# Performance work log

Hardware: AMD Instinct MI355X
Metric: run time of the kernel (lower is better)

## Reference

```python
import jax, jax.numpy as jnp
import numpy as np


def setup_inputs() -> dict:
    key = jax.random.key(0)
    ks = jax.random.split(key, 8)
    B, L, d_model = 2, 4096, 1024
    d_inner, d_state, d_conv, dt_rank = 2048, 16, 4, 64
    f = jnp.float32
    g = lambda k, shape, scale: jax.random.normal(k, shape, dtype=f) * scale
    # dt bias init: inverse-softplus of dt ~ U[log 1e-3, log 1e-1] (as in Mamba)
    dt = jnp.exp(jax.random.uniform(ks[5], (d_inner,), f) * (np.log(0.1) - np.log(0.001)) + np.log(0.001))
    dt = jnp.clip(dt, 1e-4, None)
    inv_dt = dt + jnp.log(-jnp.expm1(-dt))
    A_log = jnp.log(jnp.broadcast_to(jnp.arange(1, d_state + 1, dtype=f), (d_inner, d_state)))
    return {
        "hidden_states": jax.random.normal(ks[0], (B, L, d_model), f),
        "in_proj_w": g(ks[1], (2 * d_inner, d_model), 0.02),
        "conv_w": g(ks[2], (d_inner, d_conv), 0.1),
        "conv_b": jnp.zeros((d_inner,), f),
        "x_proj_w": g(ks[3], (dt_rank + 2 * d_state, d_inner), 0.02),
        "dt_proj_w": g(ks[4], (d_inner, dt_rank), dt_rank ** -0.5),
        "dt_proj_b": inv_dt,
        "A_log": A_log,
        "D": jnp.ones((d_inner,), f),
        "out_proj_w": g(ks[6], (d_model, d_inner), 0.02),
    }


def reference(hidden_states, in_proj_w, conv_w, conv_b, x_proj_w, dt_proj_w, dt_proj_b, A_log, D, out_proj_w):
    B_, L, _ = hidden_states.shape
    d_inner, d_conv = conv_w.shape
    dt_rank = dt_proj_w.shape[1]
    d_state = A_log.shape[1]

    # input projection -> x, z gates (B, L, d_inner) each
    xz = jnp.einsum('bld,ed->ble', hidden_states, in_proj_w)
    x, z = jnp.split(xz, 2, axis=-1)

    # causal depthwise conv1d over time + SiLU
    xc = jnp.transpose(x, (0, 2, 1))                       # (B, d_inner, L)
    kern = conv_w[:, None, :]                              # (O=d_inner, I/g=1, W)
    xc = jax.lax.conv_general_dilated(
        xc, kern, window_strides=(1,), padding=[(d_conv - 1, 0)],
        dimension_numbers=('NCH', 'OIH', 'NCH'), feature_group_count=d_inner)
    xc = xc + conv_b[None, :, None]
    x = jax.nn.silu(jnp.transpose(xc, (0, 2, 1)))          # (B, L, d_inner)

    # data-dependent SSM parameters
    x_dbl = jnp.einsum('bld,kd->blk', x, x_proj_w)         # (B, L, dt_rank+2n)
    dt, Bm, Cm = jnp.split(x_dbl, [dt_rank, dt_rank + d_state], axis=-1)
    dt = jnp.einsum('blr,dr->bld', dt, dt_proj_w)
    dt = jax.nn.softplus(dt + dt_proj_b)                   # delta_softplus + delta_bias
    A = -jnp.exp(A_log)                                    # (d_inner, d_state)

    # selective scan over the sequence dim; carry h: (B, d_inner, d_state)
    def step(h, inp):
        x_t, dt_t, B_t, C_t = inp                          # (B,d) (B,d) (B,n) (B,n)
        dA = jnp.exp(dt_t[..., None] * A)                  # (B, d, n)
        h = h * dA + (dt_t * x_t)[..., None] * B_t[:, None, :]
        y = jnp.einsum('bdn,bn->bd', h, C_t)
        return h, y

    h0 = jnp.zeros((B_, d_inner, d_state), x.dtype)
    xs = (jnp.transpose(x, (1, 0, 2)), jnp.transpose(dt, (1, 0, 2)),
          jnp.transpose(Bm, (1, 0, 2)), jnp.transpose(Cm, (1, 0, 2)))
    _, ys = jax.lax.scan(step, h0, xs)                     # ys: (L, B, d_inner)

    y = jnp.transpose(ys, (1, 0, 2)) + x * D               # skip via D
    y = y * jax.nn.silu(z)                                 # gate
    return jnp.einsum('bld,od->blo', y, out_proj_w)        # (B, L, d_model)
```

## Files before the change

kernel.cpp:

```cpp
#include <hip/hip_runtime.h>
#include <cmath>

#define CH 64
#define NC 64

typedef __bf16 bf16_t;
typedef __attribute__((ext_vector_type(8))) __bf16 bf16x8;
typedef __attribute__((ext_vector_type(4))) __bf16 bf16x4;
typedef __attribute__((ext_vector_type(4))) float f32x4;

#define GLOAD_LDS16(gp, lp)                                                     \
    __builtin_amdgcn_global_load_lds(                                           \
        (const __attribute__((address_space(1))) unsigned int*)(uintptr_t)(gp), \
        (__attribute__((address_space(3))) unsigned int*)(uintptr_t)(lp),       \
        16, 0, 0)

__global__ __launch_bounds__(256) void split5n(
    const float* __restrict__ a, bf16_t* __restrict__ ah, int n4a,
    const float* __restrict__ b, bf16_t* __restrict__ bh, int n4b,
    const float* __restrict__ c, bf16_t* __restrict__ ch, bf16_t* __restrict__ cl, int n4c,
    const float* __restrict__ d, bf16_t* __restrict__ dh, bf16_t* __restrict__ dl, int n4d,
    const float* __restrict__ e, bf16_t* __restrict__ eh, int n4e)
{
    int i = blockIdx.x * 256 + threadIdx.x;
    if (i < n4a) {
        const float4 v = ((const float4*)a)[i];
        bf16x4 hv = {(bf16_t)v.x, (bf16_t)v.y, (bf16_t)v.z, (bf16_t)v.w};
        ((bf16x4*)ah)[i] = hv;
        return;
    }
    i -= n4a;
    if (i < n4b) {
        const float4 v = ((const float4*)b)[i];
        bf16x4 hv = {(bf16_t)v.x, (bf16_t)v.y, (bf16_t)v.z, (bf16_t)v.w};
        ((bf16x4*)bh)[i] = hv;
        return;
    }
    i -= n4b;
    if (i >= n4c + n4d) {
        i -= n4c + n4d;
        if (i < n4e) {
            const float4 v = ((const float4*)e)[i];
            bf16x4 hv = {(bf16_t)v.x, (bf16_t)v.y, (bf16_t)v.z, (bf16_t)v.w};
            ((bf16x4*)eh)[i] = hv;
        }
        return;
    }
    const float* src; bf16_t* hp; bf16_t* lp;
    if (i < n4c) { src = c; hp = ch; lp = cl; }
    else         { i -= n4c; src = d; hp = dh; lp = dl; }

    const float4 v = ((const float4*)src)[i];
    const bf16_t h0 = (bf16_t)v.x, h1 = (bf16_t)v.y,
                 h2 = (bf16_t)v.z, h3 = (bf16_t)v.w;
    bf16x4 hv = {h0, h1, h2, h3};
    bf16x4 lv = {(bf16_t)(v.x - (float)h0), (bf16_t)(v.y - (float)h1),
                 (bf16_t)(v.z - (float)h2), (bf16_t)(v.w - (float)h3)};
    ((bf16x4*)hp)[i] = hv;
    ((bf16x4*)lp)[i] = lv;
}

__global__ __launch_bounds__(256) void add8_split(
    const float* __restrict__ p, float* __restrict__ o,
    bf16_t* __restrict__ dth, bf16_t* __restrict__ dtl,
    int n4, size_t stride4)
{
    const int i = blockIdx.x * 256 + threadIdx.x;
    if (i >= n4) return;
    float4 s = make_float4(0.f, 0.f, 0.f, 0.f);
#pragma unroll
    for (int k = 0; k < 8; ++k) {
        const float4 v = ((const float4*)p)[(size_t)k * stride4 + i];
        s.x += v.x; s.y += v.y; s.z += v.z; s.w += v.w;
    }
    ((float4*)o)[i] = s;

    const int col4 = i % 24;
    if (col4 < 16) {
        const int row = i / 24;
        const bf16_t h0 = (bf16_t)s.x, h1 = (bf16_t)s.y,
                     h2 = (bf16_t)s.z, h3 = (bf16_t)s.w;
        bf16x4 hv = {h0, h1, h2, h3};
        bf16x4 lv = {(bf16_t)(s.x - (float)h0), (bf16_t)(s.y - (float)h1),
                     (bf16_t)(s.z - (float)h2), (bf16_t)(s.w - (float)h3)};
        ((bf16x4*)dth)[(size_t)row * 16 + col4] = hv;
        ((bf16x4*)dtl)[(size_t)row * 16 + col4] = lv;
    }
}

__global__ __launch_bounds__(256) void in_proj_fused1(
    const bf16_t* __restrict__ Ah, const bf16_t* __restrict__ Wh,
    bf16_t* __restrict__ X, bf16_t* __restrict__ Z, int Ktot)
{
    __shared__ __align__(16) bf16_t Ash[128 * 32];
    __shared__ __align__(16) bf16_t Bsh[128 * 32];

    const int tid  = threadIdx.x;
    const int lane = tid & 63;
    const int w    = tid >> 6;
    const int wr   = (w >> 1) * 64;
    const int wc   = (w & 1) * 64;
    const int bm   = blockIdx.x * 128;
    const int by   = blockIdx.y;
    const int bnW  = by * 128;
    const int l16  = lane & 15;
    const int lhi  = lane >> 4;

    f32x4 acc[4][4];
#pragma unroll
    for (int i = 0; i < 4; ++i)
#pragma unroll
        for (int j = 0; j < 4; ++j)
#pragma unroll
            for (int r = 0; r < 4; ++r) acc[i][j][r] = 0.f;

    const int srow0 = tid >> 2;
    const int sks   = (tid & 3) << 3;
    const int ldsb0 = tid * 16;

    for (int k0 = 0; k0 < Ktot; k0 += 32) {
        __syncthreads();
#pragma unroll
        for (int call = 0; call < 2; ++call) {
            const int row = srow0 + call * 64;
            const int wb  = ldsb0 + call * 4096;
            GLOAD_LDS16(Ah + (size_t)(bm + row) * Ktot + k0 + sks, (char*)Ash + wb);
            GLOAD_LDS16(Wh + (size_t)(bnW + row) * Ktot + k0 + sks, (char*)Bsh + wb);
        }
        __syncthreads();

        bf16x8 af[4], bfr[4];
#pragma unroll
        for (int f = 0; f < 4; ++f) {
            af[f]  = *(const bf16x8*)&Ash[(wr + f * 16 + l16) * 32 + lhi * 8];
            bfr[f] = *(const bf16x8*)&Bsh[(wc + f * 16 + l16) * 32 + lhi * 8];
        }
#pragma unroll
        for (int fm = 0; fm < 4; ++fm)
#pragma unroll
            for (int fn = 0; fn < 4; ++fn)
                acc[fm][fn] = __builtin_amdgcn_mfma_f32_16x16x32_bf16(
                    af[fm], bfr[fn], acc[fm][fn], 0, 0, 0);
    }

    bf16_t* outp = (by < 16) ? X : Z;
    const int bnC = ((by < 16) ? by : (by - 16)) * 128;
#pragma unroll
    for (int fm = 0; fm < 4; ++fm) {
        const int row0 = bm + wr + fm * 16 + lhi * 4;
#pragma unroll
        for (int fn = 0; fn < 4; ++fn) {
            const int col = bnC + wc + fn * 16 + l16;
#pragma unroll
            for (int r = 0; r < 4; ++r)
                outp[(size_t)(row0 + r) * 2048 + col] = (bf16_t)acc[fm][fn][r];
        }
    }
}

__global__ __launch_bounds__(256) void gemm_mfma3dt(
    const bf16_t* __restrict__ Ah, const bf16_t* __restrict__ Al,
    const bf16_t* __restrict__ Bh, const bf16_t* __restrict__ Bl,
    bf16_t* __restrict__ C, const float* __restrict__ bias,
    int Ktot, int ldc)
{
    __shared__ __align__(16) bf16_t Ash[128 * 32];
    __shared__ __align__(16) bf16_t Asl[128 * 32];
    __shared__ __align__(16) bf16_t Bsh[128 * 32];
    __shared__ __align__(16) bf16_t Bsl[128 * 32];

    const int tid  = threadIdx.x;
    const int lane = tid & 63;
    const int w    = tid >> 6;
    const int wr   = (w >> 1) * 64;
    const int wc   = (w & 1) * 64;
    const int bm   = blockIdx.x * 128;
    const int bn   = blockIdx.y * 128;
    const int l16  = lane & 15;
    const int lhi  = lane >> 4;

    f32x4 acc[4][4];
#pragma unroll
    for (int i = 0; i < 4; ++i)
#pragma unroll
        for (int j = 0; j < 4; ++j)
#pragma unroll
            for (int r = 0; r < 4; ++r) acc[i][j][r] = 0.f;

    const int srow0 = tid >> 2;
    const int sks   = (tid & 3) << 3;
    const int ldsb0 = tid * 16;

    for (int k0 = 0; k0 < Ktot; k0 += 32) {
        __syncthreads();
#pragma unroll
        for (int call = 0; call < 2; ++call) {
            const int row = srow0 + call * 64;
            const int wb  = ldsb0 + call * 4096;
            const size_t aoff = (size_t)(bm + row) * Ktot + k0 + sks;
            const size_t boff = (size_t)(bn + row) * Ktot + k0 + sks;
            GLOAD_LDS16(Ah + aoff, (char*)Ash + wb);
            GLOAD_LDS16(Al + aoff, (char*)Asl + wb);
            GLOAD_LDS16(Bh + boff, (char*)Bsh + wb);
            GLOAD_LDS16(Bl + boff, (char*)Bsl + wb);
        }
        __syncthreads();

        bf16x8 ah[4], al[4], bh[4], bl[4];
#pragma unroll
        for (int f = 0; f < 4; ++f) {
            const int ar = (wr + f * 16 + l16) * 32 + lhi * 8;
            const int br = (wc + f * 16 + l16) * 32 + lhi * 8;
            ah[f] = *(const bf16x8*)&Ash[ar];
            al[f] = *(const bf16x8*)&Asl[ar];
            bh[f] = *(const bf16x8*)&Bsh[br];
            bl[f] = *(const bf16x8*)&Bsl[br];
        }
#pragma unroll
        for (int fm = 0; fm < 4; ++fm)
#pragma unroll
            for (int fn = 0; fn < 4; ++fn) {
                acc[fm][fn] = __builtin_amdgcn_mfma_f32_16x16x32_bf16(
                    ah[fm], bh[fn], acc[fm][fn], 0, 0, 0);
                acc[fm][fn] = __builtin_amdgcn_mfma_f32_16x16x32_bf16(
                    al[fm], bh[fn], acc[fm][fn], 0, 0, 0);
                acc[fm][fn] = __builtin_amdgcn_mfma_f32_16x16x32_bf16(
                    ah[fm], bl[fn], acc[fm][fn], 0, 0, 0);
            }
    }

#pragma unroll
    for (int fm = 0; fm < 4; ++fm) {
        const int row0 = bm + wr + fm * 16 + lhi * 4;
#pragma unroll
        for (int fn = 0; fn < 4; ++fn) {
            const int col = bn + wc + fn * 16 + l16;
#pragma unroll
            for (int r = 0; r < 4; ++r) {
                float v = acc[fm][fn][r] + bias[col];
                v = (v > 20.f) ? v : log1pf(expf(v));
                C[(size_t)(row0 + r) * ldc + col] = (bf16_t)v;
            }
        }
    }
}

__global__ __launch_bounds__(256) void gemm_mfma2x(
    const bf16_t* __restrict__ Ah,
    const bf16_t* __restrict__ Bh, const bf16_t* __restrict__ Bl,
    float* __restrict__ C, int Ktot, int Ksplit, size_t partStride)
{
    __shared__ __align__(16) bf16_t Ash[128 * 32];
    __shared__ __align__(16) bf16_t Bsh[128 * 32];
    __shared__ __align__(16) bf16_t Bsl[128 * 32];

    const int tid  = threadIdx.x;
    const int lane = tid & 63;
    const int w    = tid >> 6;
    const int wr   = (w >> 1) * 64;
    const int wc   = (w & 1) * 64;
    const int bm   = blockIdx.x * 128;
    const int l16  = lane & 15;
    const int lhi  = lane >> 4;

    f32x4 acc[4][4];
#pragma unroll
    for (int i = 0; i < 4; ++i)
#pragma unroll
        for (int j = 0; j < 4; ++j)
#pragma unroll
            for (int r = 0; r < 4; ++r) acc[i][j][r] = 0.f;

    const int srow0 = tid >> 2;
    const int sks   = (tid & 3) << 3;
    const int ldsb0 = tid * 16;

    const int kBeg = blockIdx.z * Ksplit;
    const int kEnd = kBeg + Ksplit;

    for (int k0 = kBeg; k0 < kEnd; k0 += 32) {
        __syncthreads();
#pragma unroll
        for (int call = 0; call < 2; ++call) {
            const int row  = srow0 + call * 64;
            const int brow = (row < 96) ? row : 95;
            const int wb   = ldsb0 + call * 4096;
            const size_t aoff = (size_t)(bm + row) * Ktot + k0 + sks;
            const size_t boff = (size_t)brow * Ktot + k0 + sks;
            GLOAD_LDS16(Ah + aoff, (char*)Ash + wb);
            GLOAD_LDS16(Bh + boff, (char*)Bsh + wb);
            GLOAD_LDS16(Bl + boff, (char*)Bsl + wb);
        }
        __syncthreads();

        bf16x8 ah[4], bh[4], bl[4];
#pragma unroll
        for (int f = 0; f < 4; ++f) {
            const int ar = (wr + f * 16 + l16) * 32 + lhi * 8;
            const int br = (wc + f * 16 + l16) * 32 + lhi * 8;
            ah[f] = *(const bf16x8*)&Ash[ar];
            bh[f] = *(const bf16x8*)&Bsh[br];
            bl[f] = *(const bf16x8*)&Bsl[br];
        }
#pragma unroll
        for (int fm = 0; fm < 4; ++fm)
#pragma unroll
            for (int fn = 0; fn < 4; ++fn) {
                acc[fm][fn] = __builtin_amdgcn_mfma_f32_16x16x32_bf16(
                    ah[fm], bh[fn], acc[fm][fn], 0, 0, 0);
                acc[fm][fn] = __builtin_amdgcn_mfma_f32_16x16x32_bf16(
                    ah[fm], bl[fn], acc[fm][fn], 0, 0, 0);
            }
    }

    float* Cp = C + (size_t)blockIdx.z * partStride;
#pragma unroll
    for (int fm = 0; fm < 4; ++fm) {
        const int row0 = bm + wr + fm * 16 + lhi * 4;
#pragma unroll
        for (int fn = 0; fn < 4; ++fn) {
            const int col = wc + fn * 16 + l16;
            if (col < 96) {
#pragma unroll
                for (int r = 0; r < 4; ++r)
                    Cp[(size_t)(row0 + r) * 96 + col] = acc[fm][fn][r];
            }
        }
    }
}

__global__ __launch_bounds__(256) void gemm_mfma1o128(
    const bf16_t* __restrict__ Ah, const bf16_t* __restrict__ Bh,
    float* __restrict__ C, int K, int ldc)
{
    __shared__ __align__(16) bf16_t Ash[128 * 32];
    __shared__ __align__(16) bf16_t Bsh[128 * 32];

    const int tid  = threadIdx.x;
    const int lane = tid & 63;
    const int w    = tid >> 6;
    const int wr   = (w >> 1) * 64;
    const int wc   = (w & 1) * 64;
    const int bm   = blockIdx.x * 128;
    const int bn   = blockIdx.y * 128;
    const int l16  = lane & 15;
    const int lhi  = lane >> 4;

    f32x4 acc[4][4];
#pragma unroll
    for (int i = 0; i < 4; ++i)
#pragma unroll
        for (int j = 0; j < 4; ++j)
#pragma unroll
            for (int r = 0; r < 4; ++r) acc[i][j][r] = 0.f;

    const int srow0 = tid >> 2;
    const int sks   = (tid & 3) << 3;
    const int ldsb0 = tid * 16;

    for (int k0 = 0; k0 < K; k0 += 32) {
        __syncthreads();
#pragma unroll
        for (int call = 0; call < 2; ++call) {
            const int row = srow0 + call * 64;
            const int wb  = ldsb0 + call * 4096;
            GLOAD_LDS16(Ah + (size_t)(bm + row) * K + k0 + sks, (char*)Ash + wb);
            GLOAD_LDS16(Bh + (size_t)(bn + row) * K + k0 + sks, (char*)Bsh + wb);
        }
        __syncthreads();

        bf16x8 af[4], bfr[4];
#pragma unroll
        for (int f = 0; f < 4; ++f) {
            af[f]  = *(const bf16x8*)&Ash[(wr + f * 16 + l16) * 32 + lhi * 8];
            bfr[f] = *(const bf16x8*)&Bsh[(wc + f * 16 + l16) * 32 + lhi * 8];
        }
#pragma unroll
        for (int fm = 0; fm < 4; ++fm)
#pragma unroll
            for (int fn = 0; fn < 4; ++fn)
                acc[fm][fn] = __builtin_amdgcn_mfma_f32_16x16x32_bf16(
                    af[fm], bfr[fn], acc[fm][fn], 0, 0, 0);
    }

#pragma unroll
    for (int fm = 0; fm < 4; ++fm) {
        const int row0 = bm + wr + fm * 16 + lhi * 4;
#pragma unroll
        for (int fn = 0; fn < 4; ++fn) {
            const int col = bn + wc + fn * 16 + l16;
#pragma unroll
            for (int r = 0; r < 4; ++r)
                C[(size_t)(row0 + r) * ldc + col] = acc[fm][fn][r];
        }
    }
}

__global__ __launch_bounds__(256) void conv_silu8s(
    const bf16_t* __restrict__ xin, const float* __restrict__ w,
    const float* __restrict__ bias,
    bf16_t* __restrict__ xh,
    int L, int D)
{
    const long long e8 = (long long)blockIdx.x * 256 + threadIdx.x;
    const int Dq = D >> 3;
    const int dq = (int)(e8 % Dq);
    const long long bl = e8 / Dq;
    const int l = (int)(bl % L);
    const int d = dq << 3;
    const long long base = bl * D + d;

    float t0[8], t1[8], t2[8], t3[8];
    {
        const bf16x8 v = *(const bf16x8*)&xin[base];
#pragma unroll
        for (int j = 0; j < 8; ++j) t0[j] = (float)v[j];
    }
    if (l >= 1) { const bf16x8 v = *(const bf16x8*)&xin[base - D];
#pragma unroll
        for (int j = 0; j < 8; ++j) t1[j] = (float)v[j];
    } else { for (int j = 0; j < 8; ++j) t1[j] = 0.f; }
    if (l >= 2) { const bf16x8 v = *(const bf16x8*)&xin[base - 2 * D];
#pragma unroll
        for (int j = 0; j < 8; ++j) t2[j] = (float)v[j];
    } else { for (int j = 0; j < 8; ++j) t2[j] = 0.f; }
    if (l >= 3) { const bf16x8 v = *(const bf16x8*)&xin[base - 3 * D];
#pragma unroll
        for (int j = 0; j < 8; ++j) t3[j] = (float)v[j];
    } else { for (int j = 0; j < 8; ++j) t3[j] = 0.f; }

    bf16x8 hv;
#pragma unroll
    for (int j = 0; j < 8; ++j) {
        const float4 wv = *(const float4*)&w[(d + j) * 4];
        float acc = bias[d + j];
        acc = fmaf(wv.w, t0[j], acc);
        acc = fmaf(wv.z, t1[j], acc);
        acc = fmaf(wv.y, t2[j], acc);
        acc = fmaf(wv.x, t3[j], acc);
        const float o = acc / (1.f + __expf(-acc));
        hv[j] = (bf16_t)o;
    }
    *(bf16x8*)&xh[base] = hv;
}

__global__ __launch_bounds__(256) void scan_local2(
    const bf16_t* __restrict__ xh,
    const bf16_t* __restrict__ dtb,
    const float* __restrict__ xdbl,  const float* __restrict__ A_log,
    float* __restrict__ Sbuf, float* __restrict__ Pbuf)
{
    __shared__ float Bs[CH][16];

    const int d = blockIdx.x * 256 + threadIdx.x;
    const int c = blockIdx.y;
    const int b = blockIdx.z;
    const long long rowBase = (long long)b * 4096 + (long long)c * CH;

    {
        const int e = threadIdx.x;
        const int i = e >> 2, j = (e & 3) << 2;
        *(float4*)&Bs[i][j] = *(const float4*)&xdbl[(rowBase + i) * 96 + 64 + j];
    }
    __syncthreads();

    float a[16], S[16];
#pragma unroll
    for (int n = 0; n < 16; ++n) {
        a[n] = -__expf(A_log[d * 16 + n]);
        S[n] = 0.f;
    }
    float sumdt = 0.f;

    for (int i = 0; i < CH; ++i) {
        const long long row = rowBase + i;
        const float dtv = (float)dtb[row * 2048 + d];
        const float xv  = (float)xh[row * 2048 + d];
        const float u   = dtv * xv;
        sumdt += dtv;
#pragma unroll
        for (int n = 0; n < 16; ++n) {
            const float dA = __expf(dtv * a[n]);
            S[n] = fmaf(S[n], dA, u * Bs[i][n]);
        }
    }

    const size_t base = ((((size_t)b * NC + c) * 2048) + d) * 16;
#pragma unroll
    for (int k = 0; k < 4; ++k) {
        *(float4*)&Sbuf[base + k * 4] =
            make_float4(S[k*4], S[k*4+1], S[k*4+2], S[k*4+3]);
        *(float4*)&Pbuf[base + k * 4] =
            make_float4(__expf(sumdt * a[k*4]),   __expf(sumdt * a[k*4+1]),
                        __expf(sumdt * a[k*4+2]), __expf(sumdt * a[k*4+3]));
    }
}

__global__ __launch_bounds__(256) void scan_chunk_prefix(
    float* __restrict__ Sbuf, const float* __restrict__ Pbuf)
{
    const int tid = blockIdx.x * 256 + threadIdx.x;
    const int b  = tid >> 15;
    const int dn = tid & 32767;

    float H = 0.f;
    for (int c = 0; c < NC; ++c) {
        const size_t idx = ((size_t)b * NC + c) * 32768 + dn;
        const float S = Sbuf[idx];
        const float P = Pbuf[idx];
        Sbuf[idx] = H;
        H = fmaf(P, H, S);
    }
}

__global__ __launch_bounds__(256) void scan_final2(
    const bf16_t* __restrict__ xh,
    const bf16_t* __restrict__ dtb,
    const float* __restrict__ xdbl,  const float* __restrict__ A_log,
    const float* __restrict__ Dp,    const bf16_t* __restrict__ z,
    const float* __restrict__ Hbuf,  bf16_t* __restrict__ y)
{
    __shared__ float BCs[CH][32];

    const int d = blockIdx.x * 256 + threadIdx.x;
    const int c = blockIdx.y;
    const int b = blockIdx.z;
    const long long rowBase = (long long)b * 4096 + (long long)c * CH;

#pragma unroll
    for (int k = 0; k < 2; ++k) {
        const int e = k * 256 + threadIdx.x;
        const int i = e >> 3, j = (e & 7) << 2;
        *(float4*)&BCs[i][j] = *(const float4*)&xdbl[(rowBase + i) * 96 + 64 + j];
    }
    __syncthreads();

    float a[16], h[16];
    const size_t hbase = ((((size_t)b * NC + c) * 2048) + d) * 16;
#pragma unroll
    for (int k = 0; k < 4; ++k) {
        const float4 hv = *(const float4*)&Hbuf[hbase + k * 4];
        h[k*4] = hv.x; h[k*4+1] = hv.y; h[k*4+2] = hv.z; h[k*4+3] = hv.w;
    }
#pragma unroll
    for (int n = 0; n < 16; ++n) a[n] = -__expf(A_log[d * 16 + n]);
    const float Dv = Dp[d];

    for (int i = 0; i < CH; ++i) {
        const long long row = rowBase + i;
        const float dtv = (float)dtb[row * 2048 + d];
        const float xv  = (float)xh[row * 2048 + d];
        const float u   = dtv * xv;
        float acc = 0.f;
#pragma unroll
        for (int n = 0; n < 16; ++n) {
            const float dA = __expf(dtv * a[n]);
            h[n] = fmaf(h[n], dA, u * BCs[i][n]);
            acc  = fmaf(h[n], BCs[i][16 + n], acc);
        }
        const float zv = (float)z[row * 2048 + d];
        float yv = acc + xv * Dv;
        yv = yv * (zv / (1.f + __expf(-zv)));
        y[row * 2048 + d] = (bf16_t)yv;
    }
}

extern "C" void kernel_launch(void* const* d_in, const int* in_sizes, int n_in,
                              void* d_out, int out_size, void* d_ws, size_t ws_size,
                              hipStream_t stream)
{
    const float* hidden     = (const float*)d_in[0];
    const float* in_proj_w  = (const float*)d_in[1];
    const float* conv_w     = (const float*)d_in[2];
    const float* conv_b     = (const float*)d_in[3];
    const float* x_proj_w   = (const float*)d_in[4];
    const float* dt_proj_w  = (const float*)d_in[5];
    const float* dt_proj_b  = (const float*)d_in[6];
    const float* A_log      = (const float*)d_in[7];
    const float* Dvec       = (const float*)d_in[8];
    const float* out_proj_w = (const float*)d_in[9];
    float* out = (float*)d_out;

    const int L = 4096, dinner = 2048, dmodel = 1024;
    const int M = 2 * L;

    float* z     = (float*)d_ws;
    float* xraw  = z     + (size_t)M * dinner;
    float* xconv = xraw  + (size_t)M * dinner;
    float* xdbl  = xconv + (size_t)M * dinner;
    float* Sbuf  = xdbl  + (size_t)M * 96;

    bf16_t* w1_h  = (bf16_t*)Sbuf;
    bf16_t* hid_h = (bf16_t*)xconv;
    bf16_t* zb    = (bf16_t*)z;
    bf16_t* Xb    = (bf16_t*)xraw;
    bf16_t* xc_h  = (bf16_t*)xconv;
    float*  xp_part = xraw;
    bf16_t* dtb  = (bf16_t*)xraw;
    bf16_t* dth  = (bf16_t*)Sbuf;
    bf16_t* dtl  = dth + (size_t)M * 64;
    bf16_t* wdh  = (bf16_t*)out;
    bf16_t* wdl  = wdh + (size_t)dinner * 64;
    bf16_t* xpwh = (bf16_t*)xdbl;
    bf16_t* xpwl = xpwh + (size_t)96 * dinner;
    bf16_t* w2_h = zb + (size_t)M * dinner;
    float*  Pbuf = (float*)(w2_h + (size_t)dmodel * dinner);

    const int n4a = M * dmodel / 4;
    const int n4b = 2 * dinner * dmodel / 4;
    const int n4c = dinner * 64 / 4;
    const int n4d = 96 * dinner / 4;
    const int n4e = dmodel * dinner / 4;
    split5n<<<(n4a + n4b + n4c + n4d + n4e + 255) / 256, 256, 0, stream>>>(
        hidden, hid_h, n4a,
        in_proj_w, w1_h, n4b,
        dt_proj_w, wdh, wdl, n4c,
        x_proj_w, xpwh, xpwl, n4d,
        out_proj_w, w2_h, n4e);

    in_proj_fused1<<<dim3(M / 128, 32), 256, 0, stream>>>(
        hid_h, w1_h, Xb, zb, dmodel);

    conv_silu8s<<<(M * (long long)dinner / 8) / 256, 256, 0, stream>>>(
        Xb, conv_w, conv_b, xc_h, L, dinner);

    gemm_mfma2x<<<dim3(M / 128, 1, 8), 256, 0, stream>>>(
        xc_h, xpwh, xpwl, xp_part, dinner, dinner / 8, (size_t)M * 96);
    add8_split<<<(M * 96 / 4 + 255) / 256, 256, 0, stream>>>(
        xp_part, xdbl, dth, dtl, M * 96 / 4, (size_t)M * 96 / 4);

    gemm_mfma3dt<<<dim3(M / 128, 2048 / 128), 256, 0, stream>>>(
        dth, dtl, wdh, wdl, dtb, dt_proj_b, 64, 2048);

    scan_local2<<<dim3(dinner / 256, NC, 2), 256, 0, stream>>>(
        xc_h, dtb, xdbl, A_log, Sbuf, Pbuf);
    scan_chunk_prefix<<<256, 256, 0, stream>>>(Sbuf, Pbuf);
    scan_final2<<<dim3(dinner / 256, NC, 2), 256, 0, stream>>>(
        xc_h, dtb, xdbl, A_log, Dvec, zb, Sbuf, xc_h);

    gemm_mfma1o128<<<dim3(M / 128, 1024 / 128), 256, 0, stream>>>(
        xc_h, w2_h, out, dinner, 1024);
}
```

Baseline: 439.3 us.

## Rewrite in_proj GEMM as 256x256 double-buffered 8-wave phased kernel

Replaces the 128x128 single-buffered in_proj GEMM with a 256x256 tile, 512-thread kernel. It double-buffers LDS with K=64 steps, prefetching the next tile while MFMAs run, and uses an XOR swizzle to avoid LDS bank conflicts. Compute is split into four barrier-separated phases with s_setprio so waves interleave loads and MFMA. The aim is to raise MFMA utilization and hide global-load latency, at the cost of 128KB of LDS, single-block occupancy, and more barriers.

Measured after the change: 426.0 us. 1.03x faster.

```diff
diff --git a/kernel.cpp b/kernel.cpp
--- a/kernel.cpp
+++ b/kernel.cpp
@@ -14,6 +14,8 @@
         (const __attribute__((address_space(1))) unsigned int*)(uintptr_t)(gp), \
         (__attribute__((address_space(3))) unsigned int*)(uintptr_t)(lp),       \
         16, 0, 0)
+
+#define SCHED_FENCE() __builtin_amdgcn_sched_barrier(0)
 
 __global__ __launch_bounds__(256) void split5n(
     const float* __restrict__ a, bf16_t* __restrict__ ah, int n4a,
@@ -88,69 +90,168 @@
     }
 }
 
-__global__ __launch_bounds__(256) void in_proj_fused1(
+__global__ __launch_bounds__(512, 1) void in_proj_8ph(
     const bf16_t* __restrict__ Ah, const bf16_t* __restrict__ Wh,
     bf16_t* __restrict__ X, bf16_t* __restrict__ Z, int Ktot)
 {
-    __shared__ __align__(16) bf16_t Ash[128 * 32];
-    __shared__ __align__(16) bf16_t Bsh[128 * 32];
+    __shared__ __align__(16) bf16_t lds[2][2][2][128 * 64];
 
     const int tid  = threadIdx.x;
     const int lane = tid & 63;
-    const int w    = tid >> 6;
-    const int wr   = (w >> 1) * 64;
-    const int wc   = (w & 1) * 64;
-    const int bm   = blockIdx.x * 128;
-    const int by   = blockIdx.y;
-    const int bnW  = by * 128;
+    const int wid  = tid >> 6;
+    const int wm   = wid >> 2;
+    const int wn   = wid & 3;
     const int l16  = lane & 15;
     const int lhi  = lane >> 4;
 
-    f32x4 acc[4][4];
-#pragma unroll
-    for (int i = 0; i < 4; ++i)
+    const int bm  = blockIdx.x * 256;
+    const int bnW = blockIdx.y * 256;
+
+    const int srow = tid >> 3;
+    const int scol = (tid & 7) * 8;
+    const int sflip = (srow & 4) << 2;
+
+    f32x4 acc[8][4];
+#pragma unroll
+    for (int i = 0; i < 8; ++i)
 #pragma unroll
         for (int j = 0; j < 4; ++j)
 #pragma unroll
             for (int r = 0; r < 4; ++r) acc[i][j][r] = 0.f;
 
-    const int srow0 = tid >> 2;
-    const int sks   = (tid & 3) << 3;
-    const int ldsb0 = tid * 16;
-
-    for (int k0 = 0; k0 < Ktot; k0 += 32) {
-        __syncthreads();
-#pragma unroll
-        for (int call = 0; call < 2; ++call) {
-            const int row = srow0 + call * 64;
-            const int wb  = ldsb0 + call * 4096;
-            GLOAD_LDS16(Ah + (size_t)(bm + row) * Ktot + k0 + sks, (char*)Ash + wb);
-            GLOAD_LDS16(Wh + (size_t)(bnW + row) * Ktot + k0 + sks, (char*)Bsh + wb);
-        }
-        __syncthreads();
-
-        bf16x8 af[4], bfr[4];
-#pragma unroll
-        for (int f = 0; f < 4; ++f) {
-            af[f]  = *(const bf16x8*)&Ash[(wr + f * 16 + l16) * 32 + lhi * 8];
-            bfr[f] = *(const bf16x8*)&Bsh[(wc + f * 16 + l16) * 32 + lhi * 8];
-        }
-#pragma unroll
-        for (int fm = 0; fm < 4; ++fm)
-#pragma unroll
-            for (int fn = 0; fn < 4; ++fn)
-                acc[fm][fn] = __builtin_amdgcn_mfma_f32_16x16x32_bf16(
-                    af[fm], bfr[fn], acc[fm][fn], 0, 0, 0);
-    }
-
-    bf16_t* outp = (by < 16) ? X : Z;
-    const int bnC = ((by < 16) ? by : (by - 16)) * 128;
-#pragma unroll
-    for (int fm = 0; fm < 4; ++fm) {
-        const int row0 = bm + wr + fm * 16 + lhi * 4;
+    const int NT = Ktot >> 6;
+
+    auto STAGE_TILE = [&](int pbuf, int kt) {
+        const int kc = kt * 64 + (scol ^ sflip);
+#pragma unroll
+        for (int h = 0; h < 2; ++h) {
+#pragma unroll
+            for (int j = 0; j < 2; ++j) {
+                const int row = h * 128 + j * 64 + srow;
+                char* da = (char*)&lds[pbuf][0][h][0] + (j * 512 + tid) * 16;
+                char* db = (char*)&lds[pbuf][1][h][0] + (j * 512 + tid) * 16;
+                GLOAD_LDS16(Ah + (size_t)(bm  + row) * Ktot + kc, da);
+                GLOAD_LDS16(Wh + (size_t)(bnW + row) * Ktot + kc, db);
+            }
+        }
+    };
+
+    const int rflip = (l16 & 4) << 2;
+    auto A_FRAG = [&](int p, int fm, int kk) -> bf16x8 {
+        return *(const bf16x8*)&lds[p][0][wm]
+            [(fm * 16 + l16) * 64 + ((kk * 32 + lhi * 8) ^ rflip)];
+    };
+    auto B_FRAG = [&](int p, int fn, int kk) -> bf16x8 {
+        return *(const bf16x8*)&lds[p][1][wn >> 1]
+            [((wn & 1) * 64 + fn * 16 + l16) * 64 + ((kk * 32 + lhi * 8) ^ rflip)];
+    };
+
+    STAGE_TILE(0, 0);
+    SCHED_FENCE();
+    asm volatile("s_waitcnt vmcnt(0)" ::: "memory");
+    __builtin_amdgcn_s_barrier();
+    SCHED_FENCE();
+
+    for (int kt = 0; kt < NT; ++kt) {
+        const int p  = kt & 1;
+        const int pn = p ^ 1;
+        bf16x8 a0[4][2], a1[4][2], b0[2][2], b1[2][2];
+
+#pragma unroll
+        for (int f = 0; f < 4; ++f)
+#pragma unroll
+            for (int kk = 0; kk < 2; ++kk) a0[f][kk] = A_FRAG(p, f, kk);
+#pragma unroll
+        for (int f = 0; f < 2; ++f)
+#pragma unroll
+            for (int kk = 0; kk < 2; ++kk) b0[f][kk] = B_FRAG(p, f, kk);
+        if (kt + 1 < NT) STAGE_TILE(pn, kt + 1);
+        SCHED_FENCE();
+        __builtin_amdgcn_s_barrier();
+        SCHED_FENCE();
+        __builtin_amdgcn_s_setprio(1);
+#pragma unroll
+        for (int f = 0; f < 4; ++f)
+#pragma unroll
+            for (int n = 0; n < 2; ++n)
+#pragma unroll
+                for (int kk = 0; kk < 2; ++kk)
+                    acc[f][n] = __builtin_amdgcn_mfma_f32_16x16x32_bf16(
+                        a0[f][kk], b0[n][kk], acc[f][n], 0, 0, 0);
+        __builtin_amdgcn_s_setprio(0);
+        SCHED_FENCE();
+        __builtin_amdgcn_s_barrier();
+        SCHED_FENCE();
+
+#pragma unroll
+        for (int f = 0; f < 2; ++f)
+#pragma unroll
+            for (int kk = 0; kk < 2; ++kk) b1[f][kk] = B_FRAG(p, f + 2, kk);
+        SCHED_FENCE();
+        __builtin_amdgcn_s_barrier();
+        SCHED_FENCE();
+        __builtin_amdgcn_s_setprio(1);
+#pragma unroll
+        for (int f = 0; f < 4; ++f)
+#pragma unroll
+            for (int n = 0; n < 2; ++n)
+#pragma unroll
+                for (int kk = 0; kk < 2; ++kk)
+                    acc[f][n + 2] = __builtin_amdgcn_mfma_f32_16x16x32_bf16(
+                        a0[f][kk], b1[n][kk], acc[f][n + 2], 0, 0, 0);
+        __builtin_amdgcn_s_setprio(0);
+        SCHED_FENCE();
+        __builtin_amdgcn_s_barrier();
+        SCHED_FENCE();
+
+#pragma unroll
+        for (int f = 0; f < 4; ++f)
+#pragma unroll
+            for (int kk = 0; kk < 2; ++kk) a1[f][kk] = A_FRAG(p, f + 4, kk);
+        SCHED_FENCE();
+        __builtin_amdgcn_s_barrier();
+        SCHED_FENCE();
+        __builtin_amdgcn_s_setprio(1);
+#pragma unroll
+        for (int f = 0; f < 4; ++f)
+#pragma unroll
+            for (int n = 0; n < 2; ++n)
+#pragma unroll
+                for (int kk = 0; kk < 2; ++kk)
+                    acc[f + 4][n] = __builtin_amdgcn_mfma_f32_16x16x32_bf16(
+                        a1[f][kk], b0[n][kk], acc[f + 4][n], 0, 0, 0);
+        __builtin_amdgcn_s_setprio(0);
+        SCHED_FENCE();
+        __builtin_amdgcn_s_barrier();
+        SCHED_FENCE();
+
+        SCHED_FENCE();
+        asm volatile("s_waitcnt vmcnt(0)" ::: "memory");
+        __builtin_amdgcn_s_barrier();
+        SCHED_FENCE();
+        __builtin_amdgcn_s_setprio(1);
+#pragma unroll
+        for (int f = 0; f < 4; ++f)
+#pragma unroll
+            for (int n = 0; n < 2; ++n)
+#pragma unroll
+                for (int kk = 0; kk < 2; ++kk)
+                    acc[f + 4][n + 2] = __builtin_amdgcn_mfma_f32_16x16x32_bf16(
+                        a1[f][kk], b1[n][kk], acc[f + 4][n + 2], 0, 0, 0);
+        __builtin_amdgcn_s_setprio(0);
+        SCHED_FENCE();
+        __builtin_amdgcn_s_barrier();
+        SCHED_FENCE();
+    }
+
+    bf16_t* outp = (blockIdx.y < 8) ? X : Z;
+    const int bnC = ((blockIdx.y < 8) ? blockIdx.y : (blockIdx.y - 8)) * 256;
+#pragma unroll
+    for (int fm = 0; fm < 8; ++fm) {
+        const int row0 = bm + wm * 128 + fm * 16 + lhi * 4;
 #pragma unroll
         for (int fn = 0; fn < 4; ++fn) {
-            const int col = bnC + wc + fn * 16 + l16;
+            const int col = bnC + wn * 64 + fn * 16 + l16;
 #pragma unroll
             for (int r = 0; r < 4; ++r)
                 outp[(size_t)(row0 + r) * 2048 + col] = (bf16_t)acc[fm][fn][r];
@@ -618,7 +719,7 @@
         x_proj_w, xpwh, xpwl, n4d,
         out_proj_w, w2_h, n4e);
 
-    in_proj_fused1<<<dim3(M / 128, 32), 256, 0, stream>>>(
+    in_proj_8ph<<<dim3(M / 256, 16), 512, 0, stream>>>(
         hid_h, w1_h, Xb, zb, dmodel);
 
     conv_silu8s<<<(M * (long long)dinner / 8) / 256, 256, 0, stream>>>(
```
